# Performance work log

Measured on AMD Instinct MI355X. Metric: run time of the kernel, lower is better.

Reference implementation:

```python
import jax, jax.numpy as jnp
import numpy as np

D_MODEL = 1024
NUM_HEADS = 16
HEAD_DIM = D_MODEL // NUM_HEADS


def setup_inputs() -> dict:
    key = jax.random.key(0)
    ks = jax.random.split(key, 9)
    B, L, D = 2, 2048, D_MODEL
    s = 1.0 / np.sqrt(D)
    return {
        "x": jax.random.normal(ks[0], (B, L, D), dtype=jnp.float32),
        "Wq": jax.random.normal(ks[1], (D, D), dtype=jnp.float32) * s,
        "bq": jax.random.normal(ks[2], (D,), dtype=jnp.float32) * 0.01,
        "Wk": jax.random.normal(ks[3], (D, D), dtype=jnp.float32) * s,
        "bk": jax.random.normal(ks[4], (D,), dtype=jnp.float32) * 0.01,
        "Wv": jax.random.normal(ks[5], (D, D), dtype=jnp.float32) * s,
        "bv": jax.random.normal(ks[6], (D,), dtype=jnp.float32) * 0.01,
        "Wo": jax.random.normal(ks[7], (D, D), dtype=jnp.float32) * s,
        "bo": jax.random.normal(ks[8], (D,), dtype=jnp.float32) * 0.01,
    }


def reference(x, Wq, bq, Wk, bk, Wv, bv, Wo, bo):
    B, L, D = x.shape
    H, hd = NUM_HEADS, HEAD_DIM
    # projections (torch Linear: x @ W^T + b)
    q = (x @ Wq.T + bq).reshape(B, L, H, hd).transpose(0, 2, 1, 3)  # [B,H,L,hd]
    k = (x @ Wk.T + bk).reshape(B, L, H, hd).transpose(0, 2, 1, 3)
    v = (x @ Wv.T + bv).reshape(B, L, H, hd).transpose(0, 2, 1, 3)
    scores = jnp.einsum("bhqd,bhkd->bhqk", q, k) / jnp.sqrt(jnp.float32(hd))
    attn = jax.nn.softmax(scores, axis=-1)
    ctx = jnp.einsum("bhqk,bhkd->bhqd", attn, v)  # [B,H,L,hd]
    ctx = ctx.transpose(0, 2, 1, 3).reshape(B, L, D)
    return ctx @ Wo.T + bo
```

## Files before the change

### kernel.cpp

```cpp
#include <hip/hip_runtime.h>
#include <hip/hip_bf16.h>
#include <stdint.h>

typedef __attribute__((ext_vector_type(8))) short short8;
typedef __attribute__((ext_vector_type(4))) float f32x4;
typedef __attribute__((ext_vector_type(4))) unsigned int uint4v;

#define MFMA16(a, b, c) __builtin_amdgcn_mfma_f32_16x16x32_bf16((a), (b), (c), 0, 0, 0)

#define GLDS16(ldsptr, gptr)                                                                     \
    __builtin_amdgcn_global_load_lds(                                                            \
        (const __attribute__((address_space(1))) unsigned int*)(gptr),                           \
        (__attribute__((address_space(3))) unsigned int*)(ldsptr), 16, 0, 0)

#define WAITCNT(n) asm volatile("s_waitcnt vmcnt(" #n ")" ::: "memory")

__device__ __forceinline__ unsigned short f2bf(float f) {
    union { float f; unsigned u; } v; v.f = f;
    return (unsigned short)((v.u + 0x7FFFu + ((v.u >> 16) & 1u)) >> 16);
}

__device__ __forceinline__ void kxchg(unsigned& e, unsigned& o) {
    typedef __attribute__((ext_vector_type(2))) unsigned int uint2v;
    uint2v t = __builtin_amdgcn_permlane32_swap(e, o, false, false);
    uint2v f = __builtin_amdgcn_permlane16_swap(t[0], t[1], false, false);
    e = f[0]; o = f[1];
}

__device__ __forceinline__ unsigned cvt_pk_bf16(float lo, float hi) {
    unsigned r;
    asm("v_cvt_pk_bf16_f32 %0, %1, %2" : "=v"(r) : "v"(lo), "v"(hi));
    return r;
}

__global__ void cvt_all(const float* __restrict__ x,
                        const float* __restrict__ wq, const float* __restrict__ wk,
                        const float* __restrict__ wv, const float* __restrict__ wo,
                        unsigned short* __restrict__ xb,
                        unsigned short* __restrict__ wqb, unsigned short* __restrict__ wkb,
                        unsigned short* __restrict__ wvb, unsigned short* __restrict__ wob) {
    int bid = blockIdx.x;
    const float* s; unsigned short* d; int off;
    if (bid < 4096) {
        s = x; d = xb; off = bid;
    } else {
        int w = (bid - 4096) >> 10;
        off = (bid - 4096) & 1023;
        switch (w) {
            case 0: s = wq; d = wqb; break;
            case 1: s = wk; d = wkb; break;
            case 2: s = wv; d = wvb; break;
            default: s = wo; d = wob; break;
        }
    }
    int i = off * 256 + threadIdx.x;
    float4 v = reinterpret_cast<const float4*>(s)[i];
    ushort4 o;
    o.x = f2bf(v.x); o.y = f2bf(v.y); o.z = f2bf(v.z); o.w = f2bf(v.w);
    reinterpret_cast<ushort4*>(d)[i] = o;
}

__device__ __forceinline__ void gemm_core_mfma(
    const unsigned short* __restrict__ A, const unsigned short* __restrict__ W,
    unsigned short* sl, int m0, int n0, f32x4 (&acc)[4][4])
{
    const int tid = threadIdx.x;
    const int lane = tid & 63, wid = tid >> 6;
    const int l15 = lane & 15, grp = lane >> 4;
    const int wm = (wid >> 1) * 64, wn = (wid & 1) * 64;
    const int rs_ = tid >> 3, c8 = tid & 7;

    auto stage = [&](int buf, int kt) {
        unsigned short* As = &sl[buf * 16384];
        unsigned short* Bs = &sl[buf * 16384 + 8192];
#pragma unroll
        for (int q = 0; q < 4; ++q) {
            int r = q * 32 + rs_;
            int sc = (c8 ^ (r & 7)) << 3;
            GLDS16(&As[(q * 256 + tid) * 8], &A[(size_t)(m0 + r) * 1024 + kt + sc]);
        }
#pragma unroll
        for (int q = 0; q < 4; ++q) {
            int r = q * 32 + rs_;
            int sc = (c8 ^ (r & 7)) << 3;
            GLDS16(&Bs[(q * 256 + tid) * 8], &W[(size_t)(n0 + r) * 1024 + kt + sc]);
        }
    };

    stage(0, 0);
    for (int t = 0; t < 16; ++t) {
        if (t < 15) {
            stage((t + 1) & 1, (t + 1) * 64);
            WAITCNT(8);
        } else {
            WAITCNT(0);
        }
        __builtin_amdgcn_s_barrier();
        const unsigned short* As = &sl[(t & 1) * 16384];
        const unsigned short* Bs = &sl[(t & 1) * 16384 + 8192];
#pragma unroll
        for (int ks = 0; ks < 2; ++ks) {
            short8 a[4], b[4];
#pragma unroll
            for (int i = 0; i < 4; ++i) {
                int row = wm + i * 16 + l15;
                a[i] = *reinterpret_cast<const short8*>(
                    &As[row * 64 + ((ks * 32 + grp * 8) ^ ((row & 7) << 3))]);
            }
#pragma unroll
            for (int j = 0; j < 4; ++j) {
                int row = wn + j * 16 + l15;
                b[j] = *reinterpret_cast<const short8*>(
                    &Bs[row * 64 + ((ks * 32 + grp * 8) ^ ((row & 7) << 3))]);
            }
#pragma unroll
            for (int i = 0; i < 4; ++i)
#pragma unroll
                for (int j = 0; j < 4; ++j)
                    acc[i][j] = MFMA16(a[i], b[j], acc[i][j]);
        }
        if (t < 15) __builtin_amdgcn_s_barrier();
    }
}

__global__ __launch_bounds__(256, 2) void gemm_qkv(
    const unsigned short* __restrict__ A,
    const unsigned short* __restrict__ W0, const unsigned short* __restrict__ W1,
    const unsigned short* __restrict__ W2,
    const float* __restrict__ b0, const float* __restrict__ b1, const float* __restrict__ b2,
    unsigned short* __restrict__ o0, unsigned short* __restrict__ o1,
    unsigned short* __restrict__ vt_out)
{
    __shared__ __attribute__((aligned(16))) unsigned short sl[32768];

    int id = blockIdx.x + (blockIdx.y << 3) + (blockIdx.z << 8);
    int lg = (id & 7) * 96 + (id >> 3);
    const int bx = lg & 7, by = (lg >> 3) & 31, bz = lg >> 8;

    const unsigned short* W; const float* bias; float oscale;
    if (bz == 0)      { W = W0; bias = b0; oscale = 0.18033688f; }
    else if (bz == 1) { W = W1; bias = b1; oscale = 1.0f; }
    else              { W = W2; bias = b2; oscale = 1.0f; }

    const f32x4 fz = {0.f, 0.f, 0.f, 0.f};
    f32x4 acc[4][4];
#pragma unroll
    for (int i = 0; i < 4; ++i)
#pragma unroll
        for (int j = 0; j < 4; ++j) acc[i][j] = fz;

    const int m0 = by * 128, n0 = bx * 128;
    gemm_core_mfma(A, W, sl, m0, n0, acc);

    const int tid = threadIdx.x, lane = tid & 63, wid = tid >> 6;
    const int l15 = lane & 15, grp = lane >> 4;
    const int wm = (wid >> 1) * 64, wn = (wid & 1) * 64;
    const int bb = m0 >> 11;

    if (bz < 2) {
        unsigned short* out = (bz == 0) ? o0 : o1;
#pragma unroll
        for (int j = 0; j < 4; ++j) {
            int ncol = n0 + wn + j * 16 + l15;
            float bv_ = bias[ncol];
            int h = ncol >> 6, d = ncol & 63;
#pragma unroll
            for (int i = 0; i < 4; ++i)
#pragma unroll
                for (int r = 0; r < 4; ++r) {
                    int mrow = m0 + wm + i * 16 + grp * 4 + r;
                    int ll = mrow & 2047;
                    out[(((size_t)(bb * 16 + h)) * 2048 + ll) * 64 + d] =
                        f2bf((acc[i][j][r] + bv_) * oscale);
                }
        }
    } else {
        __syncthreads();
#pragma unroll
        for (int j = 0; j < 4; ++j) {
            float bv_ = bias[n0 + wn + j * 16 + l15];
#pragma unroll
            for (int i = 0; i < 4; ++i)
#pragma unroll
                for (int r = 0; r < 4; ++r) {
                    int c = wn + j * 16 + l15;
                    int rr = wm + i * 16 + grp * 4 + r;
                    sl[c * 136 + rr] = f2bf(acc[i][j][r] + bv_);
                }
        }
        __syncthreads();
        const int llb = m0 & 2047;
#pragma unroll 4
        for (int it = 0; it < 32; ++it) {
            int c = wid * 32 + it;
            unsigned v = *reinterpret_cast<const unsigned*>(&sl[c * 136 + lane * 2]);
            int ncol = n0 + c;
            size_t row = ((size_t)(bb * 16 + (ncol >> 6))) * 64 + (ncol & 63);
            *reinterpret_cast<unsigned*>(&vt_out[row * 2048 + llb + lane * 2]) = v;
        }
    }
}

__global__ __launch_bounds__(256, 2) void gemm_out(
    const unsigned short* __restrict__ A, const unsigned short* __restrict__ W,
    const float* __restrict__ bias, float* __restrict__ out)
{
    __shared__ __attribute__((aligned(16))) unsigned short sl[32768];

    int id = blockIdx.x + (blockIdx.y << 3);
    int lg = (id & 7) * 32 + (id >> 3);
    const int bx = lg & 7, by = lg >> 3;

    const f32x4 fz = {0.f, 0.f, 0.f, 0.f};
    f32x4 acc[4][4];
#pragma unroll
    for (int i = 0; i < 4; ++i)
#pragma unroll
        for (int j = 0; j < 4; ++j) acc[i][j] = fz;

    const int m0 = by * 128, n0 = bx * 128;
    gemm_core_mfma(A, W, sl, m0, n0, acc);

    const int tid = threadIdx.x, lane = tid & 63, wid = tid >> 6;
    const int l15 = lane & 15, grp = lane >> 4;
    const int wm = (wid >> 1) * 64, wn = (wid & 1) * 64;
#pragma unroll
    for (int j = 0; j < 4; ++j) {
        int ncol = n0 + wn + j * 16 + l15;
        float bv_ = bias[ncol];
#pragma unroll
        for (int i = 0; i < 4; ++i)
#pragma unroll
            for (int r = 0; r < 4; ++r) {
                int mrow = m0 + wm + i * 16 + grp * 4 + r;
                out[(size_t)mrow * 1024 + ncol] = acc[i][j][r] + bv_;
            }
    }
}

__global__ __launch_bounds__(512, 4) void attn_kernel(
    const unsigned short* __restrict__ Q,
    const unsigned short* __restrict__ Kg,
    const unsigned short* __restrict__ VTg,
    unsigned short* __restrict__ CTX)
{
    __shared__ __attribute__((aligned(16))) unsigned short k_s[4][4096];
    __shared__ __attribute__((aligned(16))) unsigned short vt_s[4][4096];

    const int tid = threadIdx.x, lane = tid & 63, wid = tid >> 6;
    const int l15 = lane & 15, grp = lane >> 4;

    int id = blockIdx.x + (blockIdx.y << 4);
    int lg = ((id & 7) << 6) + (id >> 3);
    const int qt = lg & 15, bh = lg >> 4;

    const int rs_ = tid >> 3, c8 = tid & 7;
    const size_t kvbase = (size_t)bh * 2048 * 64;
    const size_t qbase = kvbase + (size_t)qt * 128 * 64;
    const int scv = (c8 ^ (rs_ & 7)) << 3;

    auto stageKV = [&](int t) {
        int b = t & 3;
        GLDS16(&k_s[b][tid * 8], &Kg[kvbase + (size_t)(t * 64 + rs_) * 64 + scv]);
        GLDS16(&vt_s[b][tid * 8], &VTg[kvbase + (size_t)rs_ * 2048 + t * 64 + scv]);
    };

    short8 aq[2];
    {
        const unsigned short* qp = &Q[qbase + (size_t)(wid * 16 + l15) * 64 + grp * 8];
        aq[0] = *reinterpret_cast<const short8*>(qp);
        aq[1] = *reinterpret_cast<const short8*>(qp + 32);
    }
    stageKV(0);
    stageKV(1);

    short8 ones;
#pragma unroll
    for (int i = 0; i < 8; ++i) ones[i] = (short)0x3F80;

    const f32x4 fz = {0.f, 0.f, 0.f, 0.f};
    f32x4 acc[4], acc_l = fz;
#pragma unroll
    for (int n = 0; n < 4; ++n) acc[n] = fz;

#pragma unroll 4
    for (int t = 0; t < 32; ++t) {
        if (t < 30) {
            stageKV(t + 2);
            WAITCNT(4);
        } else if (t == 30) {
            WAITCNT(2);
        } else {
            WAITCNT(0);
        }
        __builtin_amdgcn_s_barrier();
        const unsigned short* kcur = k_s[t & 3];
        const unsigned short* vcur = vt_s[t & 3];

        f32x4 st[4];
#pragma unroll
        for (int j = 0; j < 4; ++j) st[j] = fz;
#pragma unroll
        for (int ks = 0; ks < 2; ++ks)
#pragma unroll
            for (int j = 0; j < 4; ++j) {
                int row = j * 16 + l15;
                short8 bk = *reinterpret_cast<const short8*>(
                    &kcur[row * 64 + ((ks * 32 + grp * 8) ^ ((row & 7) << 3))]);
                st[j] = MFMA16(bk, aq[ks], st[j]);
            }

        unsigned pk[4][2];
#pragma unroll
        for (int j = 0; j < 4; ++j) {
            float p0 = __builtin_amdgcn_exp2f(st[j][0]);
            float p1 = __builtin_amdgcn_exp2f(st[j][1]);
            float p2 = __builtin_amdgcn_exp2f(st[j][2]);
            float p3 = __builtin_amdgcn_exp2f(st[j][3]);
            pk[j][0] = cvt_pk_bf16(p0, p1);
            pk[j][1] = cvt_pk_bf16(p2, p3);
        }

        unsigned e0 = pk[0][0], o0 = pk[1][0]; kxchg(e0, o0);
        unsigned e1 = pk[0][1], o1 = pk[1][1]; kxchg(e1, o1);
        unsigned e2 = pk[2][0], o2 = pk[3][0]; kxchg(e2, o2);
        unsigned e3 = pk[2][1], o3 = pk[3][1]; kxchg(e3, o3);
        union { uint4v u; short8 s; } ap0, ap1;
        ap0.u = (uint4v){e0, e1, o0, o1};
        ap1.u = (uint4v){e2, e3, o2, o3};

        __builtin_amdgcn_s_setprio(1);
#pragma unroll
        for (int ks = 0; ks < 2; ++ks) {
            short8 ap = ks ? ap1.s : ap0.s;
            acc_l = MFMA16(ap, ones, acc_l);
#pragma unroll
            for (int n = 0; n < 4; ++n) {
                int row = n * 16 + l15;
                short8 bv = *reinterpret_cast<const short8*>(
                    &vcur[row * 64 + ((ks * 32 + grp * 8) ^ ((row & 7) << 3))]);
                acc[n] = MFMA16(ap, bv, acc[n]);
            }
        }
        __builtin_amdgcn_s_setprio(0);
    }

    const int b = bh >> 4, h = bh & 15;
    float inv[4];
#pragma unroll
    for (int r = 0; r < 4; ++r) inv[r] = 1.0f / acc_l[r];
#pragma unroll
    for (int n = 0; n < 4; ++n)
#pragma unroll
        for (int r = 0; r < 4; ++r) {
            int qrow = qt * 128 + wid * 16 + grp * 4 + r;
            CTX[((size_t)(b * 2048 + qrow)) * 1024 + h * 64 + n * 16 + l15] =
                f2bf(acc[n][r] * inv[r]);
        }
}

extern "C" void kernel_launch(void* const* d_in, const int* in_sizes, int n_in,
                              void* d_out, int out_size, void* d_ws, size_t ws_size,
                              hipStream_t stream) {
    const float* x  = (const float*)d_in[0];
    const float* Wq = (const float*)d_in[1];
    const float* bq = (const float*)d_in[2];
    const float* Wk = (const float*)d_in[3];
    const float* bk = (const float*)d_in[4];
    const float* Wv = (const float*)d_in[5];
    const float* bv = (const float*)d_in[6];
    const float* Wo = (const float*)d_in[7];
    const float* bo = (const float*)d_in[8];
    float* out = (float*)d_out;

    char* ws = (char*)d_ws;
    unsigned short* xb  = (unsigned short*)(ws + ((size_t)0));
    unsigned short* wqb = (unsigned short*)(ws + ((size_t)8  << 20));
    unsigned short* wkb = (unsigned short*)(ws + ((size_t)10 << 20));
    unsigned short* wvb = (unsigned short*)(ws + ((size_t)12 << 20));
    unsigned short* wob = (unsigned short*)(ws + ((size_t)14 << 20));
    unsigned short* qb  = (unsigned short*)(ws + ((size_t)16 << 20));
    unsigned short* kb  = (unsigned short*)(ws + ((size_t)24 << 20));
    unsigned short* vt  = (unsigned short*)(ws + ((size_t)32 << 20));
    unsigned short* ctx = (unsigned short*)(ws + ((size_t)0));

    cvt_all<<<8192, 256, 0, stream>>>(x, Wq, Wk, Wv, Wo, xb, wqb, wkb, wvb, wob);

    gemm_qkv<<<dim3(8, 32, 3), 256, 0, stream>>>(xb, wqb, wkb, wvb, bq, bk, bv, qb, kb, vt);
    attn_kernel<<<dim3(16, 32), 512, 0, stream>>>(qb, kb, vt, ctx);
    gemm_out<<<dim3(8, 32), 256, 0, stream>>>(ctx, wob, bo, out);
}
```

Baseline: 97.69 us.

## Switch attention to 32x32 MFMA with 256-query tiles per block

Each wave in the attention kernel now handles 32 query rows using 32x32x16 bf16 MFMAs instead of 16-row 16x16x32 tiles, and each block covers 256 queries, so the grid halves. This doubles reuse of each staged K/V tile and cuts LDS reads per FLOP. The P-matrix repacking drops to a single permlane32 swap. In exchange register pressure rises (launch bounds lowered to 2) and there are only 256 blocks, which may underfill the GPU.

Result: no change. 96.75 us (-1.0%).

```diff
diff --git a/kernel.cpp b/kernel.cpp
--- a/kernel.cpp
+++ b/kernel.cpp
@@ -4,9 +4,12 @@
 
 typedef __attribute__((ext_vector_type(8))) short short8;
 typedef __attribute__((ext_vector_type(4))) float f32x4;
+typedef __attribute__((ext_vector_type(16))) float f32x16;
 typedef __attribute__((ext_vector_type(4))) unsigned int uint4v;
+typedef __attribute__((ext_vector_type(2))) unsigned int uint2v;
 
 #define MFMA16(a, b, c) __builtin_amdgcn_mfma_f32_16x16x32_bf16((a), (b), (c), 0, 0, 0)
+#define MFMA32(a, b, c) __builtin_amdgcn_mfma_f32_32x32x16_bf16((a), (b), (c), 0, 0, 0)
 
 #define GLDS16(ldsptr, gptr)                                                                     \
     __builtin_amdgcn_global_load_lds(                                                            \
@@ -18,13 +21,6 @@
 __device__ __forceinline__ unsigned short f2bf(float f) {
     union { float f; unsigned u; } v; v.f = f;
     return (unsigned short)((v.u + 0x7FFFu + ((v.u >> 16) & 1u)) >> 16);
-}
-
-__device__ __forceinline__ void kxchg(unsigned& e, unsigned& o) {
-    typedef __attribute__((ext_vector_type(2))) unsigned int uint2v;
-    uint2v t = __builtin_amdgcn_permlane32_swap(e, o, false, false);
-    uint2v f = __builtin_amdgcn_permlane16_swap(t[0], t[1], false, false);
-    e = f[0]; o = f[1];
 }
 
 __device__ __forceinline__ unsigned cvt_pk_bf16(float lo, float hi) {
@@ -238,7 +234,7 @@
     }
 }
 
-__global__ __launch_bounds__(512, 4) void attn_kernel(
+__global__ __launch_bounds__(512, 2) void attn_kernel(
     const unsigned short* __restrict__ Q,
     const unsigned short* __restrict__ Kg,
     const unsigned short* __restrict__ VTg,
@@ -248,15 +244,15 @@
     __shared__ __attribute__((aligned(16))) unsigned short vt_s[4][4096];
 
     const int tid = threadIdx.x, lane = tid & 63, wid = tid >> 6;
-    const int l15 = lane & 15, grp = lane >> 4;
-
-    int id = blockIdx.x + (blockIdx.y << 4);
-    int lg = ((id & 7) << 6) + (id >> 3);
-    const int qt = lg & 15, bh = lg >> 4;
+    const int l31 = lane & 31, h = lane >> 5;
+
+    int id = blockIdx.x + (blockIdx.y << 3);
+    int lg = ((id & 7) << 5) + (id >> 3);
+    const int qt = lg & 7, bh = lg >> 3;
 
     const int rs_ = tid >> 3, c8 = tid & 7;
     const size_t kvbase = (size_t)bh * 2048 * 64;
-    const size_t qbase = kvbase + (size_t)qt * 128 * 64;
+    const size_t qbase = kvbase + (size_t)qt * 256 * 64;
     const int scv = (c8 ^ (rs_ & 7)) << 3;
 
     auto stageKV = [&](int t) {
@@ -265,11 +261,12 @@
         GLDS16(&vt_s[b][tid * 8], &VTg[kvbase + (size_t)rs_ * 2048 + t * 64 + scv]);
     };
 
-    short8 aq[2];
+    short8 aq[4];
     {
-        const unsigned short* qp = &Q[qbase + (size_t)(wid * 16 + l15) * 64 + grp * 8];
-        aq[0] = *reinterpret_cast<const short8*>(qp);
-        aq[1] = *reinterpret_cast<const short8*>(qp + 32);
+        const unsigned short* qp = &Q[qbase + (size_t)(wid * 32 + l31) * 64 + h * 8];
+#pragma unroll
+        for (int kq = 0; kq < 4; ++kq)
+            aq[kq] = *reinterpret_cast<const short8*>(qp + kq * 16);
     }
     stageKV(0);
     stageKV(1);
@@ -278,10 +275,9 @@
 #pragma unroll
     for (int i = 0; i < 8; ++i) ones[i] = (short)0x3F80;
 
-    const f32x4 fz = {0.f, 0.f, 0.f, 0.f};
-    f32x4 acc[4], acc_l = fz;
-#pragma unroll
-    for (int n = 0; n < 4; ++n) acc[n] = fz;
+    f32x16 acc[2], acc_l;
+#pragma unroll
+    for (int i = 0; i < 16; ++i) { acc[0][i] = 0.f; acc[1][i] = 0.f; acc_l[i] = 0.f; }
 
 #pragma unroll 4
     for (int t = 0; t < 32; ++t) {
@@ -297,66 +293,68 @@
         const unsigned short* kcur = k_s[t & 3];
         const unsigned short* vcur = vt_s[t & 3];
 
-        f32x4 st[4];
-#pragma unroll
-        for (int j = 0; j < 4; ++j) st[j] = fz;
-#pragma unroll
-        for (int ks = 0; ks < 2; ++ks)
-#pragma unroll
-            for (int j = 0; j < 4; ++j) {
-                int row = j * 16 + l15;
-                short8 bk = *reinterpret_cast<const short8*>(
-                    &kcur[row * 64 + ((ks * 32 + grp * 8) ^ ((row & 7) << 3))]);
-                st[j] = MFMA16(bk, aq[ks], st[j]);
-            }
-
-        unsigned pk[4][2];
-#pragma unroll
-        for (int j = 0; j < 4; ++j) {
-            float p0 = __builtin_amdgcn_exp2f(st[j][0]);
-            float p1 = __builtin_amdgcn_exp2f(st[j][1]);
-            float p2 = __builtin_amdgcn_exp2f(st[j][2]);
-            float p3 = __builtin_amdgcn_exp2f(st[j][3]);
-            pk[j][0] = cvt_pk_bf16(p0, p1);
-            pk[j][1] = cvt_pk_bf16(p2, p3);
-        }
-
-        unsigned e0 = pk[0][0], o0 = pk[1][0]; kxchg(e0, o0);
-        unsigned e1 = pk[0][1], o1 = pk[1][1]; kxchg(e1, o1);
-        unsigned e2 = pk[2][0], o2 = pk[3][0]; kxchg(e2, o2);
-        unsigned e3 = pk[2][1], o3 = pk[3][1]; kxchg(e3, o3);
-        union { uint4v u; short8 s; } ap0, ap1;
-        ap0.u = (uint4v){e0, e1, o0, o1};
-        ap1.u = (uint4v){e2, e3, o2, o3};
+        f32x16 st[2];
+#pragma unroll
+        for (int i = 0; i < 16; ++i) { st[0][i] = 0.f; st[1][i] = 0.f; }
+#pragma unroll
+        for (int kb = 0; kb < 2; ++kb)
+#pragma unroll
+            for (int kq = 0; kq < 4; ++kq) {
+                int row = kb * 32 + l31;
+                short8 ak = *reinterpret_cast<const short8*>(
+                    &kcur[row * 64 + ((kq * 16 + h * 8) ^ ((row & 7) << 3))]);
+                st[kb] = MFMA32(ak, aq[kq], st[kb]);
+            }
+
+        unsigned pk[2][4][2];
+#pragma unroll
+        for (int kb = 0; kb < 2; ++kb)
+#pragma unroll
+            for (int g = 0; g < 4; ++g)
+#pragma unroll
+                for (int p = 0; p < 2; ++p)
+                    pk[kb][g][p] = cvt_pk_bf16(
+                        __builtin_amdgcn_exp2f(st[kb][4 * g + 2 * p]),
+                        __builtin_amdgcn_exp2f(st[kb][4 * g + 2 * p + 1]));
+
+        union { uint4v u; short8 s; } ap[4];
+#pragma unroll
+        for (int kb = 0; kb < 2; ++kb)
+#pragma unroll
+            for (int j = 0; j < 2; ++j) {
+                uint2v s0 = __builtin_amdgcn_permlane32_swap(
+                    pk[kb][2 * j][0], pk[kb][2 * j + 1][0], false, false);
+                uint2v s1 = __builtin_amdgcn_permlane32_swap(
+                    pk[kb][2 * j][1], pk[kb][2 * j + 1][1], false, false);
+                ap[2 * kb + j].u = (uint4v){s0[0], s1[0], s0[1], s1[1]};
+            }
 
         __builtin_amdgcn_s_setprio(1);
 #pragma unroll
-        for (int ks = 0; ks < 2; ++ks) {
-            short8 ap = ks ? ap1.s : ap0.s;
-            acc_l = MFMA16(ap, ones, acc_l);
-#pragma unroll
-            for (int n = 0; n < 4; ++n) {
-                int row = n * 16 + l15;
+        for (int kk = 0; kk < 4; ++kk) {
+            acc_l = MFMA32(ap[kk].s, ones, acc_l);
+#pragma unroll
+            for (int db = 0; db < 2; ++db) {
+                int row = db * 32 + l31;
                 short8 bv = *reinterpret_cast<const short8*>(
-                    &vcur[row * 64 + ((ks * 32 + grp * 8) ^ ((row & 7) << 3))]);
-                acc[n] = MFMA16(ap, bv, acc[n]);
+                    &vcur[row * 64 + ((kk * 16 + h * 8) ^ ((row & 7) << 3))]);
+                acc[db] = MFMA32(ap[kk].s, bv, acc[db]);
             }
         }
         __builtin_amdgcn_s_setprio(0);
     }
 
-    const int b = bh >> 4, h = bh & 15;
-    float inv[4];
-#pragma unroll
-    for (int r = 0; r < 4; ++r) inv[r] = 1.0f / acc_l[r];
-#pragma unroll
-    for (int n = 0; n < 4; ++n)
-#pragma unroll
-        for (int r = 0; r < 4; ++r) {
-            int qrow = qt * 128 + wid * 16 + grp * 4 + r;
-            CTX[((size_t)(b * 2048 + qrow)) * 1024 + h * 64 + n * 16 + l15] =
-                f2bf(acc[n][r] * inv[r]);
-        }
+    const int b = bh >> 4, hh = bh & 15;
+#pragma unroll
+    for (int r = 0; r < 16; ++r) {
+        int q_local = (r & 3) + 8 * (r >> 2) + 4 * h;
+        int qrow = qt * 256 + wid * 32 + q_local;
+        float inv = 1.0f / acc_l[r];
+#pragma unroll
+        for (int db = 0; db < 2; ++db)
+            CTX[((size_t)(b * 2048 + qrow)) * 1024 + hh * 64 + db * 32 + l31] =
+                f2bf(acc[db][r] * inv);
+    }
 }
 
 extern "C" void kernel_launch(void* const* d_in, const int* in_sizes, int n_in,
@@ -387,6 +385,6 @@
     cvt_all<<<8192, 256, 0, stream>>>(x, Wq, Wk, Wv, Wo, xb, wqb, wkb, wvb, wob);
 
     gemm_qkv<<<dim3(8, 32, 3), 256, 0, stream>>>(xb, wqb, wkb, wvb, bq, bk, bv, qb, kb, vt);
-    attn_kernel<<<dim3(16, 32), 512, 0, stream>>>(qb, kb, vt, ctx);
+    attn_kernel<<<dim3(8, 32), 512, 0, stream>>>(qb, kb, vt, ctx);
     gemm_out<<<dim3(8, 32), 256, 0, stream>>>(ctx, wob, bo, out);
 }
```

## Split key tiles across wave pairs in attention and reduce partials via LDS

Applied to the files above, without the earlier changes.

Each attention block now handles 64 query rows instead of 128. Its 8 waves form 4 query groups × 2 key halves: each wave computes scores for 32 of the 64 keys per tile and accumulates a partial P·V. The two halves are combined through an LDS reduction at the end, and the grid doubles to 1024 blocks for more parallelism and occupancy. The cost is that K/V tiles are loaded twice as often per query row, plus an extra sync and LDS reduction.

Result: slower. 102.8 us (+5.2%).

```diff
diff --git a/kernel.cpp b/kernel.cpp
--- a/kernel.cpp
+++ b/kernel.cpp
@@ -249,14 +249,15 @@
 
     const int tid = threadIdx.x, lane = tid & 63, wid = tid >> 6;
     const int l15 = lane & 15, grp = lane >> 4;
-
-    int id = blockIdx.x + (blockIdx.y << 4);
-    int lg = ((id & 7) << 6) + (id >> 3);
-    const int qt = lg & 15, bh = lg >> 4;
+    const int qg = wid & 3, kh = wid >> 2;
+
+    int id = blockIdx.x + (blockIdx.y << 5);
+    int lg = ((id & 7) << 7) + (id >> 3);
+    const int qt = lg & 31, bh = lg >> 5;
 
     const int rs_ = tid >> 3, c8 = tid & 7;
     const size_t kvbase = (size_t)bh * 2048 * 64;
-    const size_t qbase = kvbase + (size_t)qt * 128 * 64;
+    const size_t qbase = kvbase + (size_t)qt * 64 * 64;
     const int scv = (c8 ^ (rs_ & 7)) << 3;
 
     auto stageKV = [&](int t) {
@@ -267,7 +268,7 @@
 
     short8 aq[2];
     {
-        const unsigned short* qp = &Q[qbase + (size_t)(wid * 16 + l15) * 64 + grp * 8];
+        const unsigned short* qp = &Q[qbase + (size_t)(qg * 16 + l15) * 64 + grp * 8];
         aq[0] = *reinterpret_cast<const short8*>(qp);
         aq[1] = *reinterpret_cast<const short8*>(qp + 32);
     }
@@ -297,66 +298,81 @@
         const unsigned short* kcur = k_s[t & 3];
         const unsigned short* vcur = vt_s[t & 3];
 
-        f32x4 st[4];
-#pragma unroll
-        for (int j = 0; j < 4; ++j) st[j] = fz;
+        f32x4 st[2];
+#pragma unroll
+        for (int j2 = 0; j2 < 2; ++j2) st[j2] = fz;
 #pragma unroll
         for (int ks = 0; ks < 2; ++ks)
 #pragma unroll
-            for (int j = 0; j < 4; ++j) {
-                int row = j * 16 + l15;
+            for (int j2 = 0; j2 < 2; ++j2) {
+                int row = (kh * 2 + j2) * 16 + l15;
                 short8 bk = *reinterpret_cast<const short8*>(
                     &kcur[row * 64 + ((ks * 32 + grp * 8) ^ ((row & 7) << 3))]);
-                st[j] = MFMA16(bk, aq[ks], st[j]);
+                st[j2] = MFMA16(bk, aq[ks], st[j2]);
             }
 
-        unsigned pk[4][2];
-#pragma unroll
-        for (int j = 0; j < 4; ++j) {
-            float p0 = __builtin_amdgcn_exp2f(st[j][0]);
-            float p1 = __builtin_amdgcn_exp2f(st[j][1]);
-            float p2 = __builtin_amdgcn_exp2f(st[j][2]);
-            float p3 = __builtin_amdgcn_exp2f(st[j][3]);
-            pk[j][0] = cvt_pk_bf16(p0, p1);
-            pk[j][1] = cvt_pk_bf16(p2, p3);
+        unsigned pk[2][2];
+#pragma unroll
+        for (int j2 = 0; j2 < 2; ++j2) {
+            float p0 = __builtin_amdgcn_exp2f(st[j2][0]);
+            float p1 = __builtin_amdgcn_exp2f(st[j2][1]);
+            float p2 = __builtin_amdgcn_exp2f(st[j2][2]);
+            float p3 = __builtin_amdgcn_exp2f(st[j2][3]);
+            pk[j2][0] = cvt_pk_bf16(p0, p1);
+            pk[j2][1] = cvt_pk_bf16(p2, p3);
         }
 
         unsigned e0 = pk[0][0], o0 = pk[1][0]; kxchg(e0, o0);
         unsigned e1 = pk[0][1], o1 = pk[1][1]; kxchg(e1, o1);
-        unsigned e2 = pk[2][0], o2 = pk[3][0]; kxchg(e2, o2);
-        unsigned e3 = pk[2][1], o3 = pk[3][1]; kxchg(e3, o3);
-        union { uint4v u; short8 s; } ap0, ap1;
-        ap0.u = (uint4v){e0, e1, o0, o1};
-        ap1.u = (uint4v){e2, e3, o2, o3};
+        union { uint4v u; short8 s; } ap;
+        ap.u = (uint4v){e0, e1, o0, o1};
 
         __builtin_amdgcn_s_setprio(1);
-#pragma unroll
-        for (int ks = 0; ks < 2; ++ks) {
-            short8 ap = ks ? ap1.s : ap0.s;
-            acc_l = MFMA16(ap, ones, acc_l);
-#pragma unroll
-            for (int n = 0; n < 4; ++n) {
-                int row = n * 16 + l15;
-                short8 bv = *reinterpret_cast<const short8*>(
-                    &vcur[row * 64 + ((ks * 32 + grp * 8) ^ ((row & 7) << 3))]);
-                acc[n] = MFMA16(ap, bv, acc[n]);
+        acc_l = MFMA16(ap.s, ones, acc_l);
+#pragma unroll
+        for (int n = 0; n < 4; ++n) {
+            int row = n * 16 + l15;
+            short8 bv = *reinterpret_cast<const short8*>(
+                &vcur[row * 64 + ((kh * 32 + grp * 8) ^ ((row & 7) << 3))]);
+            acc[n] = MFMA16(ap.s, bv, acc[n]);
+        }
+        __builtin_amdgcn_s_setprio(0);
+    }
+
+    float* red = reinterpret_cast<float*>(&k_s[0][0]);
+    __syncthreads();
+    if (kh == 1) {
+        float* p = &red[((size_t)qg * 64 + lane) * 21];
+#pragma unroll
+        for (int n = 0; n < 4; ++n)
+#pragma unroll
+            for (int r = 0; r < 4; ++r) p[n * 4 + r] = acc[n][r];
+#pragma unroll
+        for (int r = 0; r < 4; ++r) p[16 + r] = acc_l[r];
+    }
+    __syncthreads();
+    if (kh == 0) {
+        const float* p = &red[((size_t)qg * 64 + lane) * 21];
+#pragma unroll
+        for (int n = 0; n < 4; ++n)
+#pragma unroll
+            for (int r = 0; r < 4; ++r) acc[n][r] += p[n * 4 + r];
+#pragma unroll
+        for (int r = 0; r < 4; ++r) acc_l[r] += p[16 + r];
+
+        const int b = bh >> 4, hh = bh & 15;
+        float inv[4];
+#pragma unroll
+        for (int r = 0; r < 4; ++r) inv[r] = 1.0f / acc_l[r];
+#pragma unroll
+        for (int n = 0; n < 4; ++n)
+#pragma unroll
+            for (int r = 0; r < 4; ++r) {
+                int qrow = qt * 64 + qg * 16 + grp * 4 + r;
+                CTX[((size_t)(b * 2048 + qrow)) * 1024 + hh * 64 + n * 16 + l15] =
+                    f2bf(acc[n][r] * inv[r]);
             }
-        }
-        __builtin_amdgcn_s_setprio(0);
-    }
-
-    const int b = bh >> 4, h = bh & 15;
-    float inv[4];
-#pragma unroll
-    for (int r = 0; r < 4; ++r) inv[r] = 1.0f / acc_l[r];
-#pragma unroll
-    for (int n = 0; n < 4; ++n)
-#pragma unroll
-        for (int r = 0; r < 4; ++r) {
-            int qrow = qt * 128 + wid * 16 + grp * 4 + r;
-            CTX[((size_t)(b * 2048 + qrow)) * 1024 + h * 64 + n * 16 + l15] =
-                f2bf(acc[n][r] * inv[r]);
-        }
+    }
 }
 
 extern "C" void kernel_launch(void* const* d_in, const int* in_sizes, int n_in,
@@ -387,6 +403,6 @@
     cvt_all<<<8192, 256, 0, stream>>>(x, Wq, Wk, Wv, Wo, xb, wqb, wkb, wvb, wob);
 
     gemm_qkv<<<dim3(8, 32, 3), 256, 0, stream>>>(xb, wqb, wkb, wvb, bq, bk, bv, qb, kb, vt);
-    attn_kernel<<<dim3(16, 32), 512, 0, stream>>>(qb, kb, vt, ctx);
+    attn_kernel<<<dim3(32, 32), 512, 0, stream>>>(qb, kb, vt, ctx);
     gemm_out<<<dim3(8, 32), 256, 0, stream>>>(ctx, wob, bo, out);
 }
```
